# Kernel tuning notes

Hardware: AMD Instinct MI355X
Metric: run time of the kernel (lower is better)

Reference implementation:

```python
import jax, jax.numpy as jnp
import numpy as np

E = 8        # n_routed_experts
TOPK = 2     # num_experts_per_tok


def setup_inputs() -> dict:
    key = jax.random.key(0)
    k0, k1, k2, k3, k4 = jax.random.split(key, 5)
    B, S, D, H = 1, 2048, 1024, 2816
    scale = 0.02
    x = jax.random.normal(k0, (B, S, D), jnp.float32)
    Wg = jax.random.normal(k1, (E, D), jnp.float32) * scale   # gate weight [E, D]
    W1 = jax.random.normal(k2, (E, H, D), jnp.float32) * scale  # up-gate proj
    W2 = jax.random.normal(k3, (E, D, H), jnp.float32) * scale  # down proj
    W3 = jax.random.normal(k4, (E, H, D), jnp.float32) * scale  # up proj
    return {"x": x, "Wg": Wg, "W1": W1, "W2": W2, "W3": W3}


def _moe_forward(x, Wg, W1, W2, W3):
    B, S, D = x.shape
    xt = x.reshape(-1, D)                      # [T, D], T = B*S
    T = xt.shape[0]
    # --- gate: logits -> softmax -> top-k, normalized top-k weights ---
    logits = xt @ Wg.T                         # [T, E]
    scores = jax.nn.softmax(logits, axis=-1)
    w, idx = jax.lax.top_k(scores, TOPK)       # [T, K]
    w = w / (w.sum(axis=-1, keepdims=True) + 1e-20)
    # combine weights per token per expert (scatter top-k weights) [T, E]
    cw = jnp.zeros((T, E), xt.dtype).at[jnp.arange(T)[:, None], idx].add(w)
    # --- per-expert SwiGLU FFN (batched over experts) ---
    h = jax.nn.silu(jnp.einsum('td,ehd->teh', xt, W1)) * jnp.einsum('td,ehd->teh', xt, W3)  # [T,E,H]
    out = jnp.einsum('teh,edh->ted', h, W2)    # [T, E, D]
    # weighted combine of selected experts (cw is zero for unselected)
    y = jnp.einsum('te,ted->td', cw, out)      # [T, D]
    return y.reshape(B, S, D)


def reference(x, Wg, W1, W2, W3):
    return _moe_forward(x, Wg, W1, W2, W3)
```

## Files before the change

### kernel.cpp

```cpp
#include <hip/hip_runtime.h>
#include <hip/hip_bf16.h>

#define T_TOK 2048
#define D_DIM 1024
#define H_DIM 2816
#define E_NUM 8
#define CAP   1024

typedef __attribute__((ext_vector_type(8))) short short8;
typedef __attribute__((ext_vector_type(4))) float floatx4;

__device__ __forceinline__ unsigned short f2bf(float f) {
    unsigned int b = __float_as_uint(f);
    b += 0x7FFFu + ((b >> 16) & 1u);
    return (unsigned short)(b >> 16);
}

__device__ __forceinline__ unsigned pk2(float lo, float hi) {
    unsigned a = __float_as_uint(lo) + 0x8000u;
    unsigned b = __float_as_uint(hi) + 0x8000u;
    return __builtin_amdgcn_perm(b, a, 0x07060302);
}

__device__ __forceinline__ short8 pack8r(float4 a, float4 b) {
    union { uint4 u; short8 s; } r;
    r.u.x = pk2(a.x, a.y);
    r.u.y = pk2(a.z, a.w);
    r.u.z = pk2(b.x, b.y);
    r.u.w = pk2(b.z, b.w);
    return r.s;
}

__device__ __forceinline__ void gl2lds16(const void* g, void* l) {
    __builtin_amdgcn_global_load_lds(
        (const __attribute__((address_space(1))) unsigned int*)g,
        (__attribute__((address_space(3))) unsigned int*)l,
        16, 0, 0);
}


__global__ __launch_bounds__(256) void k_gate2(const float* __restrict__ x,
                                               const float* __restrict__ Wg,
                                               int* __restrict__ stok,
                                               float* __restrict__ sw,
                                               int* __restrict__ counts,
                                               unsigned short* __restrict__ xg) {
    const int wave = threadIdx.x >> 6, lane = threadIdx.x & 63;
    const int t = blockIdx.x * 4 + wave;
    const float* xr = x + (size_t)t * D_DIM;
    float acc[E_NUM];
#pragma unroll
    for (int e = 0; e < E_NUM; ++e) acc[e] = 0.f;
#pragma unroll 4
    for (int i = 0; i < D_DIM / 64; ++i) {
        float xv = xr[lane + 64 * i];
#pragma unroll
        for (int e = 0; e < E_NUM; ++e) acc[e] += xv * Wg[e * D_DIM + lane + 64 * i];
    }
#pragma unroll
    for (int e = 0; e < E_NUM; ++e) {
#pragma unroll
        for (int s = 32; s > 0; s >>= 1) acc[e] += __shfl_xor(acc[e], s, 64);
    }
    int slot0 = 0, slot1 = 0;
    if (lane == 0) {
        float mx = acc[0];
#pragma unroll
        for (int e = 1; e < E_NUM; ++e) mx = fmaxf(mx, acc[e]);
        float p[E_NUM], s = 0.f;
#pragma unroll
        for (int e = 0; e < E_NUM; ++e) { p[e] = __expf(acc[e] - mx); s += p[e]; }
        int i0 = 0;
#pragma unroll
        for (int e = 1; e < E_NUM; ++e) if (p[e] > p[i0]) i0 = e;
        int i1 = (i0 == 0) ? 1 : 0;
#pragma unroll
        for (int e = 0; e < E_NUM; ++e) if (e != i0 && p[e] > p[i1]) i1 = e;
        float s0 = p[i0] / s, s1 = p[i1] / s;
        float d = s0 + s1 + 1e-20f;
        int p0 = atomicAdd(&counts[i0], 1); if (p0 >= CAP) p0 = CAP - 1;
        int p1 = atomicAdd(&counts[i1], 1); if (p1 >= CAP) p1 = CAP - 1;
        slot0 = i0 * CAP + p0;
        slot1 = i1 * CAP + p1;
        stok[slot0] = t; sw[slot0] = s0 / d;
        stok[slot1] = t; sw[slot1] = s1 / d;
    }
    slot0 = __shfl(slot0, 0, 64);
    slot1 = __shfl(slot1, 0, 64);
    const float4* xr4 = (const float4*)xr;
    ushort4* xg4 = (ushort4*)xg;
#pragma unroll
    for (int it = 0; it < 4; ++it) {
        float4 v = xr4[lane + 64 * it];
        ushort4 o;
        o.x = f2bf(v.x); o.y = f2bf(v.y); o.z = f2bf(v.z); o.w = f2bf(v.w);
        xg4[(size_t)slot0 * 256 + lane + 64 * it] = o;
        xg4[(size_t)slot1 * 256 + lane + 64 * it] = o;
    }
}

__global__ __launch_bounds__(256) void k_gemm13(const unsigned short* __restrict__ xg,
                                                const float* __restrict__ W1,
                                                const float* __restrict__ W3,
                                                const int* __restrict__ counts,
                                                unsigned short* __restrict__ U) {
    const int nt = blockIdx.x;
    const int mt = blockIdx.y;
    const int e  = blockIdx.z;
    const int cnt = min(counts[e], CAP);
    if (mt * 256 >= cnt) return;

    __shared__ __align__(16) unsigned char As[32 * 1056];
    __shared__ __align__(16) unsigned char B1s[4 * 1056];
    __shared__ __align__(16) unsigned char B3s[4 * 1056];

    const int tid = threadIdx.x, lane = tid & 63, wave = tid >> 6;
    const int fr = lane & 15, quad = lane >> 4, f7 = fr & 7, f8 = fr >> 3;

    const unsigned short* aBase = xg
        + ((size_t)e * CAP + mt * 256 + wave * 64 + (lane >> 3)) * D_DIM
        + ((lane & 7) ^ (lane >> 3)) * 8;

    const int br = tid >> 3, bc = tid & 7;
    const float* w1p = W1 + ((size_t)e * H_DIM + nt * 32 + br) * D_DIM + bc * 8;
    const float* w3p = W3 + ((size_t)e * H_DIM + nt * 32 + br) * D_DIM + bc * 8;
    const int bslot = (br >> 3) * 1056 + (br & 7) * 128 + ((bc ^ (br & 7)) << 4);

    floatx4 acc1[4][2], acc3[4][2];
#pragma unroll
    for (int m = 0; m < 4; ++m)
#pragma unroll
        for (int n = 0; n < 2; ++n) { acc1[m][n] = (floatx4)0.f; acc3[m][n] = (floatx4)0.f; }

    const int agrp = (wave * 8 + f8) * 1056 + f7 * 128;
    const int c0 = (quad ^ f7) << 4;
    const int c1 = ((4 | quad) ^ f7) << 4;

#pragma unroll 1
    for (int k0 = 0; k0 < D_DIM; k0 += 64) {
#pragma unroll
        for (int j = 0; j < 8; ++j)
            gl2lds16(aBase + (size_t)j * 8 * D_DIM + k0, As + (wave * 8 + j) * 1056);
        float4 u0 = *(const float4*)(w1p + k0);
        float4 u1 = *(const float4*)(w1p + k0 + 4);
        float4 v0 = *(const float4*)(w3p + k0);
        float4 v1 = *(const float4*)(w3p + k0 + 4);
        *(short8*)(B1s + bslot) = pack8r(u0, u1);
        *(short8*)(B3s + bslot) = pack8r(v0, v1);
        __syncthreads();

        short8 b1f[2][2], b3f[2][2];
#pragma unroll
        for (int n = 0; n < 2; ++n) {
            const int bg = (n * 2 + f8) * 1056 + f7 * 128;
            b1f[n][0] = *(const short8*)(B1s + bg + c0);
            b1f[n][1] = *(const short8*)(B1s + bg + c1);
            b3f[n][0] = *(const short8*)(B3s + bg + c0);
            b3f[n][1] = *(const short8*)(B3s + bg + c1);
        }
#pragma unroll
        for (int m = 0; m < 4; ++m) {
            const unsigned char* ab = As + agrp + m * 2112;
            short8 a0 = *(const short8*)(ab + c0);
            short8 a1 = *(const short8*)(ab + c1);
#pragma unroll
            for (int n = 0; n < 2; ++n) {
                acc1[m][n] = __builtin_amdgcn_mfma_f32_16x16x32_bf16(a0, b1f[n][0], acc1[m][n], 0, 0, 0);
                acc1[m][n] = __builtin_amdgcn_mfma_f32_16x16x32_bf16(a1, b1f[n][1], acc1[m][n], 0, 0, 0);
                acc3[m][n] = __builtin_amdgcn_mfma_f32_16x16x32_bf16(a0, b3f[n][0], acc3[m][n], 0, 0, 0);
                acc3[m][n] = __builtin_amdgcn_mfma_f32_16x16x32_bf16(a1, b3f[n][1], acc3[m][n], 0, 0, 0);
            }
        }
        __syncthreads();
    }

#pragma unroll
    for (int m = 0; m < 4; ++m) {
#pragma unroll
        for (int r = 0; r < 4; ++r) {
            int g = mt * 256 + wave * 64 + m * 16 + quad * 4 + r;
            if (g < cnt) {
                size_t rowb = ((size_t)e * CAP + g) * H_DIM + nt * 32;
#pragma unroll
                for (int n = 0; n < 2; ++n) {
                    float u1v = acc1[m][n][r], u3v = acc3[m][n][r];
                    float u = u1v / (1.f + __expf(-u1v)) * u3v;
                    U[rowb + n * 16 + fr] = f2bf(u);
                }
            }
        }
    }
}

__global__ __launch_bounds__(256) void k_gemm2(const unsigned short* __restrict__ U,
                                               const float* __restrict__ W2,
                                               const int* __restrict__ counts,
                                               const int* __restrict__ stok,
                                               const float* __restrict__ sw,
                                               float* __restrict__ y) {
    const int nt = blockIdx.x;
    const int mt = blockIdx.y;
    const int e  = blockIdx.z;
    const int cnt = min(counts[e], CAP);
    if (mt * 256 >= cnt) return;

    __shared__ __align__(16) unsigned char As[32 * 1056];
    __shared__ __align__(16) unsigned char Bs[4 * 1056];

    const int tid = threadIdx.x, lane = tid & 63, wave = tid >> 6;
    const int fr = lane & 15, quad = lane >> 4, f7 = fr & 7, f8 = fr >> 3;

    const unsigned short* aBase = U
        + ((size_t)e * CAP + mt * 256 + wave * 64 + (lane >> 3)) * H_DIM
        + ((lane & 7) ^ (lane >> 3)) * 8;

    const int br = tid >> 3, bc = tid & 7;
    const float* w2p = W2 + ((size_t)e * D_DIM + nt * 32 + br) * H_DIM + bc * 8;
    const int bslot = (br >> 3) * 1056 + (br & 7) * 128 + ((bc ^ (br & 7)) << 4);

    floatx4 acc[4][2];
#pragma unroll
    for (int m = 0; m < 4; ++m)
#pragma unroll
        for (int n = 0; n < 2; ++n) acc[m][n] = (floatx4)0.f;

    const int agrp = (wave * 8 + f8) * 1056 + f7 * 128;
    const int c0 = (quad ^ f7) << 4;
    const int c1 = ((4 | quad) ^ f7) << 4;

#pragma unroll 1
    for (int k0 = 0; k0 < H_DIM; k0 += 64) {
#pragma unroll
        for (int j = 0; j < 8; ++j)
            gl2lds16(aBase + (size_t)j * 8 * H_DIM + k0, As + (wave * 8 + j) * 1056);
        float4 u0 = *(const float4*)(w2p + k0);
        float4 u1 = *(const float4*)(w2p + k0 + 4);
        *(short8*)(Bs + bslot) = pack8r(u0, u1);
        __syncthreads();

        short8 bf[2][2];
#pragma unroll
        for (int n = 0; n < 2; ++n) {
            const int bg = (n * 2 + f8) * 1056 + f7 * 128;
            bf[n][0] = *(const short8*)(Bs + bg + c0);
            bf[n][1] = *(const short8*)(Bs + bg + c1);
        }
#pragma unroll
        for (int m = 0; m < 4; ++m) {
            const unsigned char* ab = As + agrp + m * 2112;
            short8 a0 = *(const short8*)(ab + c0);
            short8 a1 = *(const short8*)(ab + c1);
#pragma unroll
            for (int n = 0; n < 2; ++n) {
                acc[m][n] = __builtin_amdgcn_mfma_f32_16x16x32_bf16(a0, bf[n][0], acc[m][n], 0, 0, 0);
                acc[m][n] = __builtin_amdgcn_mfma_f32_16x16x32_bf16(a1, bf[n][1], acc[m][n], 0, 0, 0);
            }
        }
        __syncthreads();
    }

#pragma unroll
    for (int m = 0; m < 4; ++m) {
#pragma unroll
        for (int r = 0; r < 4; ++r) {
            int g = mt * 256 + wave * 64 + m * 16 + quad * 4 + r;
            if (g < cnt) {
                int slot = e * CAP + g;
                int t = stok[slot];
                float w = sw[slot];
                float* yr = y + (size_t)t * D_DIM + nt * 32;
#pragma unroll
                for (int n = 0; n < 2; ++n)
                    atomicAdd(&yr[n * 16 + fr], w * acc[m][n][r]);
            }
        }
    }
}

static const size_t OFF_XG   = 0;
static const size_t OFF_U    = (size_t)E_NUM * CAP * D_DIM * 2;
static const size_t OFF_STOK = OFF_U + (size_t)E_NUM * CAP * H_DIM * 2;
static const size_t OFF_SW   = OFF_STOK + (size_t)E_NUM * CAP * 4;
static const size_t OFF_META = OFF_SW + (size_t)E_NUM * CAP * 4;

extern "C" void kernel_launch(void* const* d_in, const int* in_sizes, int n_in,
                              void* d_out, int out_size, void* d_ws, size_t ws_size,
                              hipStream_t stream) {
    const float* x  = (const float*)d_in[0];
    const float* Wg = (const float*)d_in[1];
    const float* W1 = (const float*)d_in[2];
    const float* W2 = (const float*)d_in[3];
    const float* W3 = (const float*)d_in[4];
    float* y = (float*)d_out;
    char* ws = (char*)d_ws;

    unsigned short* xg = (unsigned short*)(ws + OFF_XG);
    unsigned short* U  = (unsigned short*)(ws + OFF_U);
    int*   stok   = (int*)(ws + OFF_STOK);
    float* sw     = (float*)(ws + OFF_SW);
    int*   counts = (int*)(ws + OFF_META);

    hipMemsetAsync(counts, 0, 64, stream);
    hipMemsetAsync(y, 0, (size_t)T_TOK * D_DIM * sizeof(float), stream);

    k_gate2<<<T_TOK / 4, 256, 0, stream>>>(x, Wg, stok, sw, counts, xg);
    k_gemm13<<<dim3(H_DIM / 32, CAP / 256, E_NUM), 256, 0, stream>>>(xg, W1, W3, counts, U);
    k_gemm2<<<dim3(D_DIM / 32, CAP / 256, E_NUM), 256, 0, stream>>>(U, W2, counts, stok, sw, y);
}
```

Before: 481.6 us.

## Double-buffer LDS in expert GEMMs and widen down-proj N tile to 64

Both expert GEMM kernels now double-buffer the A and B shared-memory tiles. The next K-slice's global-to-LDS copy and weight loads are issued before the MFMA work on the current slice, which removes one barrier per iteration. The down-projection kernel doubles its N tile from 32 to 64 columns, so each streamed A tile is reused across more outputs and the grid is halved. Row padding is dropped in favour of the XOR swizzle alone, and launch bounds request 2 blocks per CU. In exchange, LDS use and accumulator registers grow, which may limit occupancy.

```diff
diff --git a/kernel.cpp b/kernel.cpp
--- a/kernel.cpp
+++ b/kernel.cpp
@@ -99,20 +99,48 @@
     }
 }
 
-__global__ __launch_bounds__(256) void k_gemm13(const unsigned short* __restrict__ xg,
-                                                const float* __restrict__ W1,
-                                                const float* __restrict__ W3,
-                                                const int* __restrict__ counts,
-                                                unsigned short* __restrict__ U) {
+__device__ __forceinline__ void g13_tile(const unsigned char* Ab, const unsigned char* B1b,
+                                         const unsigned char* B3b, int agrp, int c0, int c1,
+                                         int f8, int f7,
+                                         floatx4 (&acc1)[4][2], floatx4 (&acc3)[4][2]) {
+    short8 b1f[2][2], b3f[2][2];
+#pragma unroll
+    for (int n = 0; n < 2; ++n) {
+        const int bg = (n * 2 + f8) * 1024 + f7 * 128;
+        b1f[n][0] = *(const short8*)(B1b + bg + c0);
+        b1f[n][1] = *(const short8*)(B1b + bg + c1);
+        b3f[n][0] = *(const short8*)(B3b + bg + c0);
+        b3f[n][1] = *(const short8*)(B3b + bg + c1);
+    }
+#pragma unroll
+    for (int m = 0; m < 4; ++m) {
+        const unsigned char* ab = Ab + agrp + m * 2048;
+        short8 a0 = *(const short8*)(ab + c0);
+        short8 a1 = *(const short8*)(ab + c1);
+#pragma unroll
+        for (int n = 0; n < 2; ++n) {
+            acc1[m][n] = __builtin_amdgcn_mfma_f32_16x16x32_bf16(a0, b1f[n][0], acc1[m][n], 0, 0, 0);
+            acc1[m][n] = __builtin_amdgcn_mfma_f32_16x16x32_bf16(a1, b1f[n][1], acc1[m][n], 0, 0, 0);
+            acc3[m][n] = __builtin_amdgcn_mfma_f32_16x16x32_bf16(a0, b3f[n][0], acc3[m][n], 0, 0, 0);
+            acc3[m][n] = __builtin_amdgcn_mfma_f32_16x16x32_bf16(a1, b3f[n][1], acc3[m][n], 0, 0, 0);
+        }
+    }
+}
+
+__global__ __launch_bounds__(256, 2) void k_gemm13(const unsigned short* __restrict__ xg,
+                                                   const float* __restrict__ W1,
+                                                   const float* __restrict__ W3,
+                                                   const int* __restrict__ counts,
+                                                   unsigned short* __restrict__ U) {
     const int nt = blockIdx.x;
     const int mt = blockIdx.y;
     const int e  = blockIdx.z;
     const int cnt = min(counts[e], CAP);
     if (mt * 256 >= cnt) return;
 
-    __shared__ __align__(16) unsigned char As[32 * 1056];
-    __shared__ __align__(16) unsigned char B1s[4 * 1056];
-    __shared__ __align__(16) unsigned char B3s[4 * 1056];
+    __shared__ __align__(16) unsigned char As[2][32768];
+    __shared__ __align__(16) unsigned char B1s[2][4096];
+    __shared__ __align__(16) unsigned char B3s[2][4096];
 
     const int tid = threadIdx.x, lane = tid & 63, wave = tid >> 6;
     const int fr = lane & 15, quad = lane >> 4, f7 = fr & 7, f8 = fr >> 3;
@@ -124,7 +152,7 @@
     const int br = tid >> 3, bc = tid & 7;
     const float* w1p = W1 + ((size_t)e * H_DIM + nt * 32 + br) * D_DIM + bc * 8;
     const float* w3p = W3 + ((size_t)e * H_DIM + nt * 32 + br) * D_DIM + bc * 8;
-    const int bslot = (br >> 3) * 1056 + (br & 7) * 128 + ((bc ^ (br & 7)) << 4);
+    const int bslot = (br >> 3) * 1024 + (br & 7) * 128 + ((bc ^ (br & 7)) << 4);
 
     floatx4 acc1[4][2], acc3[4][2];
 #pragma unroll
@@ -132,47 +160,43 @@
 #pragma unroll
         for (int n = 0; n < 2; ++n) { acc1[m][n] = (floatx4)0.f; acc3[m][n] = (floatx4)0.f; }
 
-    const int agrp = (wave * 8 + f8) * 1056 + f7 * 128;
+    const int agrp = (wave * 8 + f8) * 1024 + f7 * 128;
     const int c0 = (quad ^ f7) << 4;
     const int c1 = ((4 | quad) ^ f7) << 4;
 
+#pragma unroll
+    for (int j = 0; j < 8; ++j)
+        gl2lds16(aBase + (size_t)j * 8 * D_DIM, As[0] + (wave * 8 + j) * 1024);
+    {
+        float4 u0 = *(const float4*)(w1p);
+        float4 u1 = *(const float4*)(w1p + 4);
+        float4 v0 = *(const float4*)(w3p);
+        float4 v1 = *(const float4*)(w3p + 4);
+        *(short8*)(B1s[0] + bslot) = pack8r(u0, u1);
+        *(short8*)(B3s[0] + bslot) = pack8r(v0, v1);
+    }
+    __syncthreads();
+
+    int cur = 0;
 #pragma unroll 1
-    for (int k0 = 0; k0 < D_DIM; k0 += 64) {
+    for (int t = 0; t < D_DIM / 64 - 1; ++t) {
+        const int kn = (t + 1) * 64;
 #pragma unroll
         for (int j = 0; j < 8; ++j)
-            gl2lds16(aBase + (size_t)j * 8 * D_DIM + k0, As + (wave * 8 + j) * 1056);
-        float4 u0 = *(const float4*)(w1p + k0);
-        float4 u1 = *(const float4*)(w1p + k0 + 4);
-        float4 v0 = *(const float4*)(w3p + k0);
-        float4 v1 = *(const float4*)(w3p + k0 + 4);
-        *(short8*)(B1s + bslot) = pack8r(u0, u1);
-        *(short8*)(B3s + bslot) = pack8r(v0, v1);
+            gl2lds16(aBase + (size_t)j * 8 * D_DIM + kn, As[cur ^ 1] + (wave * 8 + j) * 1024);
+        float4 u0 = *(const float4*)(w1p + kn);
+        float4 u1 = *(const float4*)(w1p + kn + 4);
+        float4 v0 = *(const float4*)(w3p + kn);
+        float4 v1 = *(const float4*)(w3p + kn + 4);
+
+        g13_tile(As[cur], B1s[cur], B3s[cur], agrp, c0, c1, f8, f7, acc1, acc3);
+
+        *(short8*)(B1s[cur ^ 1] + bslot) = pack8r(u0, u1);
+        *(short8*)(B3s[cur ^ 1] + bslot) = pack8r(v0, v1);
         __syncthreads();
-
-        short8 b1f[2][2], b3f[2][2];
-#pragma unroll
-        for (int n = 0; n < 2; ++n) {
-            const int bg = (n * 2 + f8) * 1056 + f7 * 128;
-            b1f[n][0] = *(const short8*)(B1s + bg + c0);
-            b1f[n][1] = *(const short8*)(B1s + bg + c1);
-            b3f[n][0] = *(const short8*)(B3s + bg + c0);
-            b3f[n][1] = *(const short8*)(B3s + bg + c1);
-        }
-#pragma unroll
-        for (int m = 0; m < 4; ++m) {
-            const unsigned char* ab = As + agrp + m * 2112;
-            short8 a0 = *(const short8*)(ab + c0);
-            short8 a1 = *(const short8*)(ab + c1);
-#pragma unroll
-            for (int n = 0; n < 2; ++n) {
-                acc1[m][n] = __builtin_amdgcn_mfma_f32_16x16x32_bf16(a0, b1f[n][0], acc1[m][n], 0, 0, 0);
-                acc1[m][n] = __builtin_amdgcn_mfma_f32_16x16x32_bf16(a1, b1f[n][1], acc1[m][n], 0, 0, 0);
-                acc3[m][n] = __builtin_amdgcn_mfma_f32_16x16x32_bf16(a0, b3f[n][0], acc3[m][n], 0, 0, 0);
-                acc3[m][n] = __builtin_amdgcn_mfma_f32_16x16x32_bf16(a1, b3f[n][1], acc3[m][n], 0, 0, 0);
-            }
-        }
-        __syncthreads();
-    }
+        cur ^= 1;
+    }
+    g13_tile(As[cur], B1s[cur], B3s[cur], agrp, c0, c1, f8, f7, acc1, acc3);
 
 #pragma unroll
     for (int m = 0; m < 4; ++m) {
@@ -192,20 +216,43 @@
     }
 }
 
-__global__ __launch_bounds__(256) void k_gemm2(const unsigned short* __restrict__ U,
-                                               const float* __restrict__ W2,
-                                               const int* __restrict__ counts,
-                                               const int* __restrict__ stok,
-                                               const float* __restrict__ sw,
-                                               float* __restrict__ y) {
+__device__ __forceinline__ void g2_tile(const unsigned char* Ab, const unsigned char* Bb,
+                                        int agrp, int c0, int c1, int f8, int f7,
+                                        floatx4 (&acc)[4][4]) {
+    short8 bf[4][2];
+#pragma unroll
+    for (int n = 0; n < 4; ++n) {
+        const int bg = (n * 2 + f8) * 1024 + f7 * 128;
+        bf[n][0] = *(const short8*)(Bb + bg + c0);
+        bf[n][1] = *(const short8*)(Bb + bg + c1);
+    }
+#pragma unroll
+    for (int m = 0; m < 4; ++m) {
+        const unsigned char* ab = Ab + agrp + m * 2048;
+        short8 a0 = *(const short8*)(ab + c0);
+        short8 a1 = *(const short8*)(ab + c1);
+#pragma unroll
+        for (int n = 0; n < 4; ++n) {
+            acc[m][n] = __builtin_amdgcn_mfma_f32_16x16x32_bf16(a0, bf[n][0], acc[m][n], 0, 0, 0);
+            acc[m][n] = __builtin_amdgcn_mfma_f32_16x16x32_bf16(a1, bf[n][1], acc[m][n], 0, 0, 0);
+        }
+    }
+}
+
+__global__ __launch_bounds__(256, 2) void k_gemm2(const unsigned short* __restrict__ U,
+                                                  const float* __restrict__ W2,
+                                                  const int* __restrict__ counts,
+                                                  const int* __restrict__ stok,
+                                                  const float* __restrict__ sw,
+                                                  float* __restrict__ y) {
     const int nt = blockIdx.x;
     const int mt = blockIdx.y;
     const int e  = blockIdx.z;
     const int cnt = min(counts[e], CAP);
     if (mt * 256 >= cnt) return;
 
-    __shared__ __align__(16) unsigned char As[32 * 1056];
-    __shared__ __align__(16) unsigned char Bs[4 * 1056];
+    __shared__ __align__(16) unsigned char As[2][32768];
+    __shared__ __align__(16) unsigned char Bs[2][8192];
 
     const int tid = threadIdx.x, lane = tid & 63, wave = tid >> 6;
     const int fr = lane & 15, quad = lane >> 4, f7 = fr & 7, f8 = fr >> 3;
@@ -215,49 +262,54 @@
         + ((lane & 7) ^ (lane >> 3)) * 8;
 
     const int br = tid >> 3, bc = tid & 7;
-    const float* w2p = W2 + ((size_t)e * D_DIM + nt * 32 + br) * H_DIM + bc * 8;
-    const int bslot = (br >> 3) * 1056 + (br & 7) * 128 + ((bc ^ (br & 7)) << 4);
-
-    floatx4 acc[4][2];
+    const float* w2p0 = W2 + ((size_t)e * D_DIM + nt * 64 + br) * H_DIM + bc * 8;
+    const float* w2p1 = w2p0 + (size_t)32 * H_DIM;
+    const int bslot0 = (br >> 3) * 1024 + (br & 7) * 128 + ((bc ^ (br & 7)) << 4);
+    const int bslot1 = bslot0 + 4096;
+
+    floatx4 acc[4][4];
 #pragma unroll
     for (int m = 0; m < 4; ++m)
 #pragma unroll
-        for (int n = 0; n < 2; ++n) acc[m][n] = (floatx4)0.f;
-
-    const int agrp = (wave * 8 + f8) * 1056 + f7 * 128;
+        for (int n = 0; n < 4; ++n) acc[m][n] = (floatx4)0.f;
+
+    const int agrp = (wave * 8 + f8) * 1024 + f7 * 128;
     const int c0 = (quad ^ f7) << 4;
     const int c1 = ((4 | quad) ^ f7) << 4;
 
+#pragma unroll
+    for (int j = 0; j < 8; ++j)
+        gl2lds16(aBase + (size_t)j * 8 * H_DIM, As[0] + (wave * 8 + j) * 1024);
+    {
+        float4 u0 = *(const float4*)(w2p0);
+        float4 u1 = *(const float4*)(w2p0 + 4);
+        float4 v0 = *(const float4*)(w2p1);
+        float4 v1 = *(const float4*)(w2p1 + 4);
+        *(short8*)(Bs[0] + bslot0) = pack8r(u0, u1);
+        *(short8*)(Bs[0] + bslot1) = pack8r(v0, v1);
+    }
+    __syncthreads();
+
+    int cur = 0;
 #pragma unroll 1
-    for (int k0 = 0; k0 < H_DIM; k0 += 64) {
+    for (int t = 0; t < H_DIM / 64 - 1; ++t) {
+        const int kn = (t + 1) * 64;
 #pragma unroll
         for (int j = 0; j < 8; ++j)
-            gl2lds16(aBase + (size_t)j * 8 * H_DIM + k0, As + (wave * 8 + j) * 1056);
-        float4 u0 = *(const float4*)(w2p + k0);
-        float4 u1 = *(const float4*)(w2p + k0 + 4);
-        *(short8*)(Bs + bslot) = pack8r(u0, u1);
+            gl2lds16(aBase + (size_t)j * 8 * H_DIM + kn, As[cur ^ 1] + (wave * 8 + j) * 1024);
+        float4 u0 = *(const float4*)(w2p0 + kn);
+        float4 u1 = *(const float4*)(w2p0 + kn + 4);
+        float4 v0 = *(const float4*)(w2p1 + kn);
+        float4 v1 = *(const float4*)(w2p1 + kn + 4);
+
+        g2_tile(As[cur], Bs[cur], agrp, c0, c1, f8, f7, acc);
+
+        *(short8*)(Bs[cur ^ 1] + bslot0) = pack8r(u0, u1);
+        *(short8*)(Bs[cur ^ 1] + bslot1) = pack8r(v0, v1);
         __syncthreads();
-
-        short8 bf[2][2];
-#pragma unroll
-        for (int n = 0; n < 2; ++n) {
-            const int bg = (n * 2 + f8) * 1056 + f7 * 128;
-            bf[n][0] = *(const short8*)(Bs + bg + c0);
-            bf[n][1] = *(const short8*)(Bs + bg + c1);
-        }
-#pragma unroll
-        for (int m = 0; m < 4; ++m) {
-            const unsigned char* ab = As + agrp + m * 2112;
-            short8 a0 = *(const short8*)(ab + c0);
-            short8 a1 = *(const short8*)(ab + c1);
-#pragma unroll
-            for (int n = 0; n < 2; ++n) {
-                acc[m][n] = __builtin_amdgcn_mfma_f32_16x16x32_bf16(a0, bf[n][0], acc[m][n], 0, 0, 0);
-                acc[m][n] = __builtin_amdgcn_mfma_f32_16x16x32_bf16(a1, bf[n][1], acc[m][n], 0, 0, 0);
-            }
-        }
-        __syncthreads();
-    }
+        cur ^= 1;
+    }
+    g2_tile(As[cur], Bs[cur], agrp, c0, c1, f8, f7, acc);
 
 #pragma unroll
     for (int m = 0; m < 4; ++m) {
@@ -268,9 +320,9 @@
                 int slot = e * CAP + g;
                 int t = stok[slot];
                 float w = sw[slot];
-                float* yr = y + (size_t)t * D_DIM + nt * 32;
-#pragma unroll
-                for (int n = 0; n < 2; ++n)
+                float* yr = y + (size_t)t * D_DIM + nt * 64;
+#pragma unroll
+                for (int n = 0; n < 4; ++n)
                     atomicAdd(&yr[n * 16 + fr], w * acc[m][n][r]);
             }
         }
@@ -305,5 +357,5 @@
 
     k_gate2<<<T_TOK / 4, 256, 0, stream>>>(x, Wg, stok, sw, counts, xg);
     k_gemm13<<<dim3(H_DIM / 32, CAP / 256, E_NUM), 256, 0, stream>>>(xg, W1, W3, counts, U);
-    k_gemm2<<<dim3(D_DIM / 32, CAP / 256, E_NUM), 256, 0, stream>>>(U, W2, counts, stok, sw, y);
-}
+    k_gemm2<<<dim3(D_DIM / 64, CAP / 256, E_NUM), 256, 0, stream>>>(U, W2, counts, stok, sw, y);
+}
```

Result: no change. 481.6 us (+0.0%).

## Software-pipeline expert GEMM loops and widen down-proj N tile to 64

Applied to the files above, without the earlier changes.

Restructures both expert GEMM main loops into a two-stage software pipeline. The next A tile is issued via global-to-LDS loads and the weight tile two steps ahead is prefetched into registers while the current MFMAs run, with explicit waitcnt and barrier placement. The down-projection kernel's N tile grows from 32 to 64 columns, halving its grid and A-tile reloads but doubling accumulator registers. LDS row padding is removed and occupancy is hinted at 2 blocks per CU. The main risks are a race on the single-buffered A tile and register pressure from the larger accumulators.

```diff
diff --git a/kernel.cpp b/kernel.cpp
--- a/kernel.cpp
+++ b/kernel.cpp
@@ -6,6 +6,9 @@
 #define H_DIM 2816
 #define E_NUM 8
 #define CAP   1024
+
+#define NT13  (D_DIM / 64)
+#define NT2   (H_DIM / 64)
 
 typedef __attribute__((ext_vector_type(8))) short short8;
 typedef __attribute__((ext_vector_type(4))) float floatx4;
@@ -37,6 +40,11 @@
         (__attribute__((address_space(3))) unsigned int*)l,
         16, 0, 0);
 }
+
+#define WAIT_LGKM0 asm volatile("s_waitcnt lgkmcnt(0)" ::: "memory")
+#define WAIT_VM(N) asm volatile("s_waitcnt vmcnt(" #N ")" ::: "memory")
+#define SBAR       __builtin_amdgcn_s_barrier()
+#define SCHED0     __builtin_amdgcn_sched_barrier(0)
 
 
 __global__ __launch_bounds__(256) void k_gate2(const float* __restrict__ x,
@@ -99,20 +107,68 @@
     }
 }
 
-__global__ __launch_bounds__(256) void k_gemm13(const unsigned short* __restrict__ xg,
-                                                const float* __restrict__ W1,
-                                                const float* __restrict__ W3,
-                                                const int* __restrict__ counts,
-                                                unsigned short* __restrict__ U) {
+#define G13_STEP(T, P0, P1, P2, P3, Q0, Q1, Q2, Q3)                                   \
+{                                                                                      \
+    short8 a[4][2], b1[2][2], b3[2][2];                                                \
+    _Pragma("unroll") for (int m = 0; m < 4; ++m) {                                    \
+        const unsigned char* ab = As + agrp + m * 2048;                                \
+        a[m][0] = *(const short8*)(ab + c0);                                           \
+        a[m][1] = *(const short8*)(ab + c1);                                           \
+    }                                                                                  \
+    _Pragma("unroll") for (int n = 0; n < 2; ++n) {                                    \
+        const int bg = (n * 2 + f8) * 1024 + f7 * 128;                                 \
+        b1[n][0] = *(const short8*)(B1s + bg + c0);                                    \
+        b1[n][1] = *(const short8*)(B1s + bg + c1);                                    \
+        b3[n][0] = *(const short8*)(B3s + bg + c0);                                    \
+        b3[n][1] = *(const short8*)(B3s + bg + c1);                                    \
+    }                                                                                  \
+    WAIT_LGKM0; SCHED0;                                                                \
+    SBAR; SCHED0;                                    \
+    if ((T) + 1 < NT_) {                                                               \
+        const int kn = ((T) + 1) * 64;                                                 \
+        _Pragma("unroll") for (int j = 0; j < 8; ++j)                                  \
+            gl2lds16(aBase + (size_t)j * 8 * LDK_ + kn, As + (wave * 8 + j) * 1024);   \
+    }                                                                                  \
+    SCHED0;                                                                            \
+    if ((T) + 2 < NT_) {                                                               \
+        const int k2 = ((T) + 2) * 64;                                                 \
+        Q0 = *(const float4*)(w1p + k2);                                               \
+        Q1 = *(const float4*)(w1p + k2 + 4);                                           \
+        Q2 = *(const float4*)(w3p + k2);                                               \
+        Q3 = *(const float4*)(w3p + k2 + 4);                                           \
+    }                                                                                  \
+    SCHED0;                                                                            \
+    _Pragma("unroll") for (int m = 0; m < 4; ++m) {                                    \
+        _Pragma("unroll") for (int n = 0; n < 2; ++n) {                                \
+            acc1[m][n] = __builtin_amdgcn_mfma_f32_16x16x32_bf16(a[m][0], b1[n][0], acc1[m][n], 0, 0, 0); \
+            acc1[m][n] = __builtin_amdgcn_mfma_f32_16x16x32_bf16(a[m][1], b1[n][1], acc1[m][n], 0, 0, 0); \
+            acc3[m][n] = __builtin_amdgcn_mfma_f32_16x16x32_bf16(a[m][0], b3[n][0], acc3[m][n], 0, 0, 0); \
+            acc3[m][n] = __builtin_amdgcn_mfma_f32_16x16x32_bf16(a[m][1], b3[n][1], acc3[m][n], 0, 0, 0); \
+        }                                                                              \
+    }                                                                                  \
+    if ((T) + 1 < NT_) {                                                               \
+        *(short8*)(B1s + bslot) = pack8r(P0, P1);                                      \
+        *(short8*)(B3s + bslot) = pack8r(P2, P3);                                      \
+        if ((T) + 2 < NT_) { WAIT_VM(4); } else { WAIT_VM(0); }                        \
+        WAIT_LGKM0; SCHED0;                                                            \
+        SBAR; SCHED0;                                          \
+    }                                                                                  \
+}
+
+__global__ __launch_bounds__(256, 2) void k_gemm13(const unsigned short* __restrict__ xg,
+                                                   const float* __restrict__ W1,
+                                                   const float* __restrict__ W3,
+                                                   const int* __restrict__ counts,
+                                                   unsigned short* __restrict__ U) {
     const int nt = blockIdx.x;
     const int mt = blockIdx.y;
     const int e  = blockIdx.z;
     const int cnt = min(counts[e], CAP);
     if (mt * 256 >= cnt) return;
 
-    __shared__ __align__(16) unsigned char As[32 * 1056];
-    __shared__ __align__(16) unsigned char B1s[4 * 1056];
-    __shared__ __align__(16) unsigned char B3s[4 * 1056];
+    __shared__ __align__(16) unsigned char As[32768];
+    __shared__ __align__(16) unsigned char B1s[4096];
+    __shared__ __align__(16) unsigned char B3s[4096];
 
     const int tid = threadIdx.x, lane = tid & 63, wave = tid >> 6;
     const int fr = lane & 15, quad = lane >> 4, f7 = fr & 7, f8 = fr >> 3;
@@ -124,7 +180,7 @@
     const int br = tid >> 3, bc = tid & 7;
     const float* w1p = W1 + ((size_t)e * H_DIM + nt * 32 + br) * D_DIM + bc * 8;
     const float* w3p = W3 + ((size_t)e * H_DIM + nt * 32 + br) * D_DIM + bc * 8;
-    const int bslot = (br >> 3) * 1056 + (br & 7) * 128 + ((bc ^ (br & 7)) << 4);
+    const int bslot = (br >> 3) * 1024 + (br & 7) * 128 + ((bc ^ (br & 7)) << 4);
 
     floatx4 acc1[4][2], acc3[4][2];
 #pragma unroll
@@ -132,47 +188,40 @@
 #pragma unroll
         for (int n = 0; n < 2; ++n) { acc1[m][n] = (floatx4)0.f; acc3[m][n] = (floatx4)0.f; }
 
-    const int agrp = (wave * 8 + f8) * 1056 + f7 * 128;
+    const int agrp = (wave * 8 + f8) * 1024 + f7 * 128;
     const int c0 = (quad ^ f7) << 4;
     const int c1 = ((4 | quad) ^ f7) << 4;
 
+    float4 pA0, pA1, pA2, pA3, qA0, qA1, qA2, qA3;
+    pA0 = *(const float4*)(w1p);
+    pA1 = *(const float4*)(w1p + 4);
+    pA2 = *(const float4*)(w3p);
+    pA3 = *(const float4*)(w3p + 4);
+    SCHED0;
+#pragma unroll
+    for (int j = 0; j < 8; ++j)
+        gl2lds16(aBase + (size_t)j * 8 * D_DIM, As + (wave * 8 + j) * 1024);
+    SCHED0;
+    qA0 = *(const float4*)(w1p + 64);
+    qA1 = *(const float4*)(w1p + 68);
+    qA2 = *(const float4*)(w3p + 64);
+    qA3 = *(const float4*)(w3p + 68);
+    SCHED0;
+    *(short8*)(B1s + bslot) = pack8r(pA0, pA1);
+    *(short8*)(B3s + bslot) = pack8r(pA2, pA3);
+    WAIT_VM(4);
+    WAIT_LGKM0; SCHED0;
+    SBAR; SCHED0;
+
+#define NT_  NT13
+#define LDK_ D_DIM
 #pragma unroll 1
-    for (int k0 = 0; k0 < D_DIM; k0 += 64) {
-#pragma unroll
-        for (int j = 0; j < 8; ++j)
-            gl2lds16(aBase + (size_t)j * 8 * D_DIM + k0, As + (wave * 8 + j) * 1056);
-        float4 u0 = *(const float4*)(w1p + k0);
-        float4 u1 = *(const float4*)(w1p + k0 + 4);
-        float4 v0 = *(const float4*)(w3p + k0);
-        float4 v1 = *(const float4*)(w3p + k0 + 4);
-        *(short8*)(B1s + bslot) = pack8r(u0, u1);
-        *(short8*)(B3s + bslot) = pack8r(v0, v1);
-        __syncthreads();
-
-        short8 b1f[2][2], b3f[2][2];
-#pragma unroll
-        for (int n = 0; n < 2; ++n) {
-            const int bg = (n * 2 + f8) * 1056 + f7 * 128;
-            b1f[n][0] = *(const short8*)(B1s + bg + c0);
-            b1f[n][1] = *(const short8*)(B1s + bg + c1);
-            b3f[n][0] = *(const short8*)(B3s + bg + c0);
-            b3f[n][1] = *(const short8*)(B3s + bg + c1);
-        }
-#pragma unroll
-        for (int m = 0; m < 4; ++m) {
-            const unsigned char* ab = As + agrp + m * 2112;
-            short8 a0 = *(const short8*)(ab + c0);
-            short8 a1 = *(const short8*)(ab + c1);
-#pragma unroll
-            for (int n = 0; n < 2; ++n) {
-                acc1[m][n] = __builtin_amdgcn_mfma_f32_16x16x32_bf16(a0, b1f[n][0], acc1[m][n], 0, 0, 0);
-                acc1[m][n] = __builtin_amdgcn_mfma_f32_16x16x32_bf16(a1, b1f[n][1], acc1[m][n], 0, 0, 0);
-                acc3[m][n] = __builtin_amdgcn_mfma_f32_16x16x32_bf16(a0, b3f[n][0], acc3[m][n], 0, 0, 0);
-                acc3[m][n] = __builtin_amdgcn_mfma_f32_16x16x32_bf16(a1, b3f[n][1], acc3[m][n], 0, 0, 0);
-            }
-        }
-        __syncthreads();
-    }
+    for (int t = 0; t < NT13; t += 2) {
+        G13_STEP(t,     qA0, qA1, qA2, qA3, pA0, pA1, pA2, pA3);
+        G13_STEP(t + 1, pA0, pA1, pA2, pA3, qA0, qA1, qA2, qA3);
+    }
+#undef NT_
+#undef LDK_
 
 #pragma unroll
     for (int m = 0; m < 4; ++m) {
@@ -192,20 +241,64 @@
     }
 }
 
-__global__ __launch_bounds__(256) void k_gemm2(const unsigned short* __restrict__ U,
-                                               const float* __restrict__ W2,
-                                               const int* __restrict__ counts,
-                                               const int* __restrict__ stok,
-                                               const float* __restrict__ sw,
-                                               float* __restrict__ y) {
+#define G2_STEP(T, P0, P1, P2, P3, Q0, Q1, Q2, Q3)                                     \
+{                                                                                      \
+    short8 a[4][2], bf[4][2];                                                          \
+    _Pragma("unroll") for (int m = 0; m < 4; ++m) {                                    \
+        const unsigned char* ab = As + agrp + m * 2048;                                \
+        a[m][0] = *(const short8*)(ab + c0);                                           \
+        a[m][1] = *(const short8*)(ab + c1);                                           \
+    }                                                                                  \
+    _Pragma("unroll") for (int n = 0; n < 4; ++n) {                                    \
+        const int bg = (n * 2 + f8) * 1024 + f7 * 128;                                 \
+        bf[n][0] = *(const short8*)(Bs + bg + c0);                                     \
+        bf[n][1] = *(const short8*)(Bs + bg + c1);                                     \
+    }                                                                                  \
+    WAIT_LGKM0; SCHED0;                                                                \
+    SBAR; SCHED0;                                                                      \
+    if ((T) + 1 < NT2) {                                                               \
+        const int kn = ((T) + 1) * 64;                                                 \
+        _Pragma("unroll") for (int j = 0; j < 8; ++j)                                  \
+            gl2lds16(aBase + (size_t)j * 8 * H_DIM + kn, As + (wave * 8 + j) * 1024);  \
+    }                                                                                  \
+    SCHED0;                                                                            \
+    if ((T) + 2 < NT2) {                                                               \
+        const int k2 = ((T) + 2) * 64;                                                 \
+        Q0 = *(const float4*)(w2p0 + k2);                                              \
+        Q1 = *(const float4*)(w2p0 + k2 + 4);                                          \
+        Q2 = *(const float4*)(w2p1 + k2);                                              \
+        Q3 = *(const float4*)(w2p1 + k2 + 4);                                          \
+    }                                                                                  \
+    SCHED0;                                                                            \
+    _Pragma("unroll") for (int m = 0; m < 4; ++m) {                                    \
+        _Pragma("unroll") for (int n = 0; n < 4; ++n) {                                \
+            acc[m][n] = __builtin_amdgcn_mfma_f32_16x16x32_bf16(a[m][0], bf[n][0], acc[m][n], 0, 0, 0); \
+            acc[m][n] = __builtin_amdgcn_mfma_f32_16x16x32_bf16(a[m][1], bf[n][1], acc[m][n], 0, 0, 0); \
+        }                                                                              \
+    }                                                                                  \
+    if ((T) + 1 < NT2) {                                                               \
+        *(short8*)(Bs + bslot0) = pack8r(P0, P1);                                      \
+        *(short8*)(Bs + bslot1) = pack8r(P2, P3);                                      \
+        if ((T) + 2 < NT2) { WAIT_VM(4); } else { WAIT_VM(0); }                        \
+        WAIT_LGKM0; SCHED0;                                                            \
+        SBAR; SCHED0;                                                                  \
+    }                                                                                  \
+}
+
+__global__ __launch_bounds__(256, 2) void k_gemm2(const unsigned short* __restrict__ U,
+                                                  const float* __restrict__ W2,
+                                                  const int* __restrict__ counts,
+                                                  const int* __restrict__ stok,
+                                                  const float* __restrict__ sw,
+                                                  float* __restrict__ y) {
     const int nt = blockIdx.x;
     const int mt = blockIdx.y;
     const int e  = blockIdx.z;
     const int cnt = min(counts[e], CAP);
     if (mt * 256 >= cnt) return;
 
-    __shared__ __align__(16) unsigned char As[32 * 1056];
-    __shared__ __align__(16) unsigned char Bs[4 * 1056];
+    __shared__ __align__(16) unsigned char As[32768];
+    __shared__ __align__(16) unsigned char Bs[8192];
 
     const int tid = threadIdx.x, lane = tid & 63, wave = tid >> 6;
     const int fr = lane & 15, quad = lane >> 4, f7 = fr & 7, f8 = fr >> 3;
@@ -215,48 +308,46 @@
         + ((lane & 7) ^ (lane >> 3)) * 8;
 
     const int br = tid >> 3, bc = tid & 7;
-    const float* w2p = W2 + ((size_t)e * D_DIM + nt * 32 + br) * H_DIM + bc * 8;
-    const int bslot = (br >> 3) * 1056 + (br & 7) * 128 + ((bc ^ (br & 7)) << 4);
-
-    floatx4 acc[4][2];
+    const float* w2p0 = W2 + ((size_t)e * D_DIM + nt * 64 + br) * H_DIM + bc * 8;
+    const float* w2p1 = w2p0 + (size_t)32 * H_DIM;
+    const int bslot0 = (br >> 3) * 1024 + (br & 7) * 128 + ((bc ^ (br & 7)) << 4);
+    const int bslot1 = bslot0 + 4096;
+
+    floatx4 acc[4][4];
 #pragma unroll
     for (int m = 0; m < 4; ++m)
 #pragma unroll
-        for (int n = 0; n < 2; ++n) acc[m][n] = (floatx4)0.f;
-
-    const int agrp = (wave * 8 + f8) * 1056 + f7 * 128;
+        for (int n = 0; n < 4; ++n) acc[m][n] = (floatx4)0.f;
+
+    const int agrp = (wave * 8 + f8) * 1024 + f7 * 128;
     const int c0 = (quad ^ f7) << 4;
     const int c1 = ((4 | quad) ^ f7) << 4;
 
+    float4 pA0, pA1, pA2, pA3, qA0, qA1, qA2, qA3;
+    pA0 = *(const float4*)(w2p0);
+    pA1 = *(const float4*)(w2p0 + 4);
+    pA2 = *(const float4*)(w2p1);
+    pA3 = *(const float4*)(w2p1 + 4);
+    SCHED0;
+#pragma unroll
+    for (int j = 0; j < 8; ++j)
+        gl2lds16(aBase + (size_t)j * 8 * H_DIM, As + (wave * 8 + j) * 1024);
+    SCHED0;
+    qA0 = *(const float4*)(w2p0 + 64);
+    qA1 = *(const float4*)(w2p0 + 68);
+    qA2 = *(const float4*)(w2p1 + 64);
+    qA3 = *(const float4*)(w2p1 + 68);
+    SCHED0;
+    *(short8*)(Bs + bslot0) = pack8r(pA0, pA1);
+    *(short8*)(Bs + bslot1) = pack8r(pA2, pA3);
+    WAIT_VM(4);
+    WAIT_LGKM0; SCHED0;
+    SBAR; SCHED0;
+
 #pragma unroll 1
-    for (int k0 = 0; k0 < H_DIM; k0 += 64) {
-#pragma unroll
-        for (int j = 0; j < 8; ++j)
-            gl2lds16(aBase + (size_t)j * 8 * H_DIM + k0, As + (wave * 8 + j) * 1056);
-        float4 u0 = *(const float4*)(w2p + k0);
-        float4 u1 = *(const float4*)(w2p + k0 + 4);
-        *(short8*)(Bs + bslot) = pack8r(u0, u1);
-        __syncthreads();
-
-        short8 bf[2][2];
-#pragma unroll
-        for (int n = 0; n < 2; ++n) {
-            const int bg = (n * 2 + f8) * 1056 + f7 * 128;
-            bf[n][0] = *(const short8*)(Bs + bg + c0);
-            bf[n][1] = *(const short8*)(Bs + bg + c1);
-        }
-#pragma unroll
-        for (int m = 0; m < 4; ++m) {
-            const unsigned char* ab = As + agrp + m * 2112;
-            short8 a0 = *(const short8*)(ab + c0);
-            short8 a1 = *(const short8*)(ab + c1);
-#pragma unroll
-            for (int n = 0; n < 2; ++n) {
-                acc[m][n] = __builtin_amdgcn_mfma_f32_16x16x32_bf16(a0, bf[n][0], acc[m][n], 0, 0, 0);
-                acc[m][n] = __builtin_amdgcn_mfma_f32_16x16x32_bf16(a1, bf[n][1], acc[m][n], 0, 0, 0);
-            }
-        }
-        __syncthreads();
+    for (int t = 0; t < NT2; t += 2) {
+        G2_STEP(t,     qA0, qA1, qA2, qA3, pA0, pA1, pA2, pA3);
+        G2_STEP(t + 1, pA0, pA1, pA2, pA3, qA0, qA1, qA2, qA3);
     }
 
 #pragma unroll
@@ -268,9 +359,9 @@
                 int slot = e * CAP + g;
                 int t = stok[slot];
                 float w = sw[slot];
-                float* yr = y + (size_t)t * D_DIM + nt * 32;
-#pragma unroll
-                for (int n = 0; n < 2; ++n)
+                float* yr = y + (size_t)t * D_DIM + nt * 64;
+#pragma unroll
+                for (int n = 0; n < 4; ++n)
                     atomicAdd(&yr[n * 16 + fr], w * acc[m][n][r]);
             }
         }
@@ -305,5 +396,5 @@
 
     k_gate2<<<T_TOK / 4, 256, 0, stream>>>(x, Wg, stok, sw, counts, xg);
     k_gemm13<<<dim3(H_DIM / 32, CAP / 256, E_NUM), 256, 0, stream>>>(xg, W1, W3, counts, U);
-    k_gemm2<<<dim3(D_DIM / 32, CAP / 256, E_NUM), 256, 0, stream>>>(U, W2, counts, stok, sw, y);
-}
+    k_gemm2<<<dim3(D_DIM / 64, CAP / 256, E_NUM), 256, 0, stream>>>(U, W2, counts, stok, sw, y);
+}
```

Result: faster. 430.6 us (-10.6%).
